# Kernel optimization log

Measured on AMD Instinct MI355X. Metric: run time of the kernel, lower is better.

Reference implementation:

```python
import jax, jax.numpy as jnp
import numpy as np

B, N, FEAT, HID = 1024, 128, 512, 256


def setup_inputs() -> dict:
    key = jax.random.key(0)
    k1, k2, k3, k4, k5, k6 = jax.random.split(key, 6)
    x = jax.random.normal(k1, (B, FEAT), dtype=jnp.float32)
    labels = jax.random.randint(k2, (B,), 0, N, dtype=jnp.int64)
    W_proj = jax.random.normal(k3, (FEAT, HID), dtype=jnp.float32) / np.sqrt(FEAT)
    b_proj = jax.random.normal(k4, (HID,), dtype=jnp.float32) * 0.01
    means = jax.random.normal(k5, (N, HID), dtype=jnp.float32)
    # inverse covariances must be SPD so sqrt(dist_sq) is real
    A = jax.random.normal(k6, (N, HID, HID), dtype=jnp.float32)
    inv_covs = jnp.einsum('nij,nkj->nik', A, A) / HID + 0.1 * jnp.eye(HID, dtype=jnp.float32)
    return {"x": x, "labels": labels, "W_proj": W_proj, "b_proj": b_proj,
            "means": means, "inv_covs": inv_covs}


def reference(x, labels, W_proj, b_proj, means, inv_covs):
    b = x.shape[0]
    n = means.shape[0]
    x_proj = x @ W_proj + b_proj                       # (b, hid)
    delta = x_proj[:, None, :] - means[None, :, :]     # (b, n, hid)
    # batched Mahalanobis quadratic form
    dist_sq = jnp.einsum('bni,nij,bnj->bn', delta, inv_covs, delta)
    distmat = jnp.sqrt(dist_sq + 1e-12)                # (b, n)
    center_mask = (labels[:, None] == jnp.arange(n)[None, :]).astype(distmat.dtype)
    loss = jnp.clip(distmat * center_mask, 1e-12, 1e12).sum() / b
    return loss, distmat
```

## Files before the change

kernel.cpp:

```cpp
#include <hip/hip_runtime.h>
#include <hip/hip_bf16.h>

#define B_    1024
#define N_    128
#define FEAT_ 512
#define HID_  256

typedef __bf16 bf16x8 __attribute__((ext_vector_type(8)));
typedef float  f32x4  __attribute__((ext_vector_type(4)));

__device__ __forceinline__ unsigned int f2bf(float f) {
    unsigned int u = __float_as_uint(f);
    u += 0x7fffu + ((u >> 16) & 1u);
    return u >> 16;
}
__device__ __forceinline__ unsigned int pack2(float a, float b) {
    return f2bf(a) | (f2bf(b) << 16);
}

__global__ __launch_bounds__(256) void prep_kernel(
    const float* __restrict__ x, const float* __restrict__ W,
    const float* __restrict__ bias, const float* __restrict__ means,
    const float* __restrict__ invcov,
    float* __restrict__ xp, unsigned short* __restrict__ xbf,
    unsigned short* __restrict__ Mbf, float* __restrict__ v2,
    float* __restrict__ cpart)
{
    const int t = threadIdx.x;
    if (blockIdx.x < 256) {
        __shared__ float xs[4][FEAT_];
        const int b0 = blockIdx.x * 4;
        {
            const float4* xsrc = (const float4*)(x + (size_t)b0 * FEAT_);
            const float4 v0 = xsrc[t];
            const float4 v1 = xsrc[t + 256];
            ((float4*)&xs[0][0])[t]       = v0;
            ((float4*)&xs[0][0])[t + 256] = v1;
        }
        __syncthreads();
        const int h = t;
        const float bb = bias[h];
        float a0 = bb, a1 = bb, a2 = bb, a3 = bb;
        #pragma unroll 8
        for (int f = 0; f < FEAT_; ++f) {
            const float w = W[(size_t)f * HID_ + h];
            a0 += xs[0][f] * w;
            a1 += xs[1][f] * w;
            a2 += xs[2][f] * w;
            a3 += xs[3][f] * w;
        }
        xp [(size_t)(b0 + 0) * HID_ + h] = a0;
        xp [(size_t)(b0 + 1) * HID_ + h] = a1;
        xp [(size_t)(b0 + 2) * HID_ + h] = a2;
        xp [(size_t)(b0 + 3) * HID_ + h] = a3;
        xbf[(size_t)(b0 + 0) * HID_ + h] = (unsigned short)f2bf(a0);
        xbf[(size_t)(b0 + 1) * HID_ + h] = (unsigned short)f2bf(a1);
        xbf[(size_t)(b0 + 2) * HID_ + h] = (unsigned short)f2bf(a2);
        xbf[(size_t)(b0 + 3) * HID_ + h] = (unsigned short)f2bf(a3);
    } else {
        __shared__ float sv[16][33];
        __shared__ float sw[2];
        const int cb = blockIdx.x - 256;
        const int n  = cb >> 4;
        const int jg = cb & 15;
        const float* Mn = invcov + (size_t)n * (HID_ * HID_) + (size_t)jg * 16 * HID_;
        const float* mu = means + (size_t)n * HID_;
        unsigned short* Mb = Mbf + (size_t)n * (HID_ * HID_) + (size_t)jg * 16 * HID_;
        const int gc = t & 31;
        const int r0 = t >> 5;
        const float4 mk0 = *(const float4*)(mu + gc * 8);
        const float4 mk1 = *(const float4*)(mu + gc * 8 + 4);
        #pragma unroll
        for (int i = 0; i < 2; ++i) {
            const int row = r0 + i * 8;
            const float* src = Mn + (size_t)row * HID_ + gc * 8;
            const float4 a = *(const float4*)src;
            const float4 b = *(const float4*)(src + 4);
            const int g2 = gc ^ ((row & 7) << 2);
            *(uint4*)(Mb + (size_t)row * HID_ + g2 * 8) =
                make_uint4(pack2(a.x, a.y), pack2(a.z, a.w), pack2(b.x, b.y), pack2(b.z, b.w));
            sv[row][gc] = a.x * mk0.x + a.y * mk0.y + a.z * mk0.z + a.w * mk0.w
                        + b.x * mk1.x + b.y * mk1.y + b.z * mk1.z + b.w * mk1.w;
        }
        __syncthreads();
        if (t < 128) {
            const int row = t >> 3;
            const int i0  = (t & 7) * 4;
            float v = sv[row][i0] + sv[row][i0 + 1] + sv[row][i0 + 2] + sv[row][i0 + 3];
            v += __shfl_xor(v, 1);
            v += __shfl_xor(v, 2);
            v += __shfl_xor(v, 4);
            const int j = jg * 16 + row;
            if ((t & 7) == 0) v2[(size_t)n * HID_ + j] = 2.f * v;
            float cc = ((t & 7) == 0) ? v * mu[j] : 0.f;
            cc += __shfl_xor(cc, 8);
            cc += __shfl_xor(cc, 16);
            cc += __shfl_xor(cc, 32);
            if ((t & 63) == 0) sw[t >> 6] = cc;
        }
        __syncthreads();
        if (t == 0) cpart[cb] = sw[0] + sw[1];
    }
}

__global__ __launch_bounds__(512, 4) void dist_kernel(
    const float* __restrict__ xp, const unsigned short* __restrict__ xbf,
    const unsigned short* __restrict__ Mbf, const float* __restrict__ v2,
    float* __restrict__ p)
{
    extern __shared__ unsigned short Ms[];

    const int tid  = threadIdx.x;
    const int bh   = blockIdx.x;
    const int jh   = blockIdx.y;
    const int n    = blockIdx.z;
    const int wave = tid >> 6;
    const int lane = tid & 63;
    const int q    = lane >> 4;
    const int l    = lane & 15;

    const unsigned short* src = Mbf + (size_t)n * (HID_ * HID_) + (size_t)jh * 32768;
    #pragma unroll
    for (int i = 0; i < 8; ++i) {
        const int c = i * 8 + wave;
        __builtin_amdgcn_global_load_lds(
            (const __attribute__((address_space(1))) unsigned int*)(src + (size_t)c * 512 + lane * 8),
            (__attribute__((address_space(3))) unsigned int*)&Ms[c * 512],
            16, 0, 0);
    }

    bf16x8 afrag[2][8];
    #pragma unroll
    for (int rb = 0; rb < 2; ++rb) {
        const unsigned short* xr = xbf + (size_t)(bh * 256 + wave * 32 + rb * 16 + l) * HID_;
        #pragma unroll
        for (int kk = 0; kk < 8; ++kk)
            afrag[rb][kk] = *(const bf16x8*)(xr + kk * 32 + q * 8);
    }
    float v2l[8];
    #pragma unroll
    for (int ct = 0; ct < 8; ++ct)
        v2l[ct] = v2[(size_t)n * HID_ + jh * 128 + ct * 16 + l];

    __syncthreads();

    float part[8];
    #pragma unroll
    for (int i = 0; i < 8; ++i) part[i] = 0.f;

    const size_t xbase = (size_t)(bh * 256 + wave * 32 + q * 4) * HID_ + jh * 128 + l;

    #pragma unroll
    for (int ct = 0; ct < 8; ++ct) {
        float xl[8];
        #pragma unroll
        for (int rb = 0; rb < 2; ++rb)
            #pragma unroll
            for (int r = 0; r < 4; ++r)
                xl[rb * 4 + r] = xp[xbase + (size_t)(rb * 16 + r) * HID_ + ct * 16];

        f32x4 acc0 = {0.f,0.f,0.f,0.f}, acc1 = {0.f,0.f,0.f,0.f};
        #pragma unroll
        for (int kk = 0; kk < 8; ++kk) {
            const bf16x8 bfrag = *(const bf16x8*)&Ms[(ct * 16 + l) * HID_ +
                                                     (((kk * 4 + q) ^ ((l & 7) << 2)) << 3)];
            acc0 = __builtin_amdgcn_mfma_f32_16x16x32_bf16(afrag[0][kk], bfrag, acc0, 0, 0, 0);
            acc1 = __builtin_amdgcn_mfma_f32_16x16x32_bf16(afrag[1][kk], bfrag, acc1, 0, 0, 0);
        }
        const float vv = v2l[ct];
        #pragma unroll
        for (int r = 0; r < 4; ++r) {
            part[r]     += (acc0[r] - vv) * xl[r];
            part[4 + r] += (acc1[r] - vv) * xl[4 + r];
        }
    }

    #pragma unroll
    for (int i = 0; i < 8; ++i) {
        float v = part[i];
        v += __shfl_xor(v, 1);
        v += __shfl_xor(v, 2);
        v += __shfl_xor(v, 4);
        v += __shfl_xor(v, 8);
        part[i] = v;
    }
    if (l == 0) {
        float* pb = p + (size_t)jh * (B_ * N_);
        #pragma unroll
        for (int i = 0; i < 8; ++i) {
            const int row = bh * 256 + wave * 32 + (i >> 2) * 16 + q * 4 + (i & 3);
            pb[(size_t)row * N_ + n] = part[i];
        }
    }
}

__global__ __launch_bounds__(256) void finalize_kernel(
    const float* __restrict__ p, const float* __restrict__ cpart,
    float* __restrict__ out)
{
    __shared__ float sc[128];
    const int t = threadIdx.x;
    if (t < 128) {
        float s = 0.f;
        #pragma unroll
        for (int g = 0; g < 16; ++g) s += cpart[t * 16 + g];
        sc[t] = s;
    }
    __syncthreads();
    const int i = blockIdx.x * 256 + t;
    const int n = i & (N_ - 1);
    out[1 + i] = sqrtf(p[i] + p[B_ * N_ + i] + sc[n] + 1e-12f);
}

__global__ __launch_bounds__(1024) void loss_kernel(
    const float* __restrict__ distmat, const int* __restrict__ labels,
    float* __restrict__ out)
{
    __shared__ float red[16];
    const int b = threadIdx.x;
    float s = distmat[(size_t)b * N_ + labels[b]];
    #pragma unroll
    for (int m = 1; m <= 32; m <<= 1) s += __shfl_xor(s, m);
    if ((b & 63) == 0) red[b >> 6] = s;
    __syncthreads();
    if (b == 0) {
        float t = 0.f;
        #pragma unroll
        for (int i = 0; i < 16; ++i) t += red[i];
        out[0] = t / (float)B_ + (float)(N_ - 1) * 1e-12f;
    }
}

extern "C" void kernel_launch(void* const* d_in, const int* in_sizes, int n_in,
                              void* d_out, int out_size, void* d_ws, size_t ws_size,
                              hipStream_t stream) {
    const float* x      = (const float*)d_in[0];
    const int*   labels = (const int*)d_in[1];
    const float* W      = (const float*)d_in[2];
    const float* bias   = (const float*)d_in[3];
    const float* means  = (const float*)d_in[4];
    const float* invcov = (const float*)d_in[5];
    float* out = (float*)d_out;

    char* ws = (char*)d_ws;
    unsigned short* Mbf   = (unsigned short*)(ws);
    float*          xp    = (float*)         (ws + 16777216);
    unsigned short* xbf   = (unsigned short*)(ws + 17825792);
    float*          v2    = (float*)         (ws + 18350080);
    float*          cpart = (float*)         (ws + 18481152);
    float*          p     = (float*)         (ws + 18489344);

    constexpr int DIST_LDS = 128 * HID_ * 2;
    (void)hipFuncSetAttribute((const void*)dist_kernel,
                              hipFuncAttributeMaxDynamicSharedMemorySize, DIST_LDS);

    prep_kernel<<<dim3(2304), 256, 0, stream>>>(x, W, bias, means, invcov,
                                                xp, xbf, Mbf, v2, cpart);
    dist_kernel<<<dim3(4, 2, N_), 512, DIST_LDS, stream>>>(xp, xbf, Mbf, v2, p);
    finalize_kernel<<<dim3((B_ * N_) / 256), 256, 0, stream>>>(p, cpart, out);
    loss_kernel<<<1, 1024, 0, stream>>>(out + 1, labels, out);
}
```

Measured before the change: 157.9 us.

## Fuse loss reduction into finalize, widen prep blocks and double-buffer projection loads

Removes the separate loss kernel: finalize now does the masked label sum per block and accumulates it into out[0] with atomicAdd, and prep seeds out[0] with the clip constant. The prep kernel moves to 512-thread blocks. The projection part handles 8 rows per block with float4 W loads double-buffered in registers, and the inv-cov conversion part processes 32 rows per block. This cuts one launch and should improve load efficiency in the projection, but float atomics make the loss summation order nondeterministic.

```diff
diff --git a/kernel.cpp b/kernel.cpp
--- a/kernel.cpp
+++ b/kernel.cpp
@@ -18,61 +18,77 @@
     return f2bf(a) | (f2bf(b) << 16);
 }
 
-__global__ __launch_bounds__(256) void prep_kernel(
+__global__ __launch_bounds__(512) void prep_kernel(
     const float* __restrict__ x, const float* __restrict__ W,
     const float* __restrict__ bias, const float* __restrict__ means,
     const float* __restrict__ invcov,
     float* __restrict__ xp, unsigned short* __restrict__ xbf,
     unsigned short* __restrict__ Mbf, float* __restrict__ v2,
-    float* __restrict__ cpart)
+    float* __restrict__ cpart, float* __restrict__ out)
 {
     const int t = threadIdx.x;
-    if (blockIdx.x < 256) {
-        __shared__ float xs[4][FEAT_];
-        const int b0 = blockIdx.x * 4;
+    if (blockIdx.x < 128) {
+        __shared__ float xs[8][FEAT_];
+        const int b0 = blockIdx.x * 8;
         {
             const float4* xsrc = (const float4*)(x + (size_t)b0 * FEAT_);
-            const float4 v0 = xsrc[t];
-            const float4 v1 = xsrc[t + 256];
-            ((float4*)&xs[0][0])[t]       = v0;
-            ((float4*)&xs[0][0])[t + 256] = v1;
-        }
+            ((float4*)&xs[0][0])[t]       = xsrc[t];
+            ((float4*)&xs[0][0])[t + 512] = xsrc[t + 512];
+        }
+        if (blockIdx.x == 0 && t == 0) out[0] = (float)(N_ - 1) * 1e-12f;
         __syncthreads();
-        const int h = t;
-        const float bb = bias[h];
-        float a0 = bb, a1 = bb, a2 = bb, a3 = bb;
-        #pragma unroll 8
-        for (int f = 0; f < FEAT_; ++f) {
-            const float w = W[(size_t)f * HID_ + h];
-            a0 += xs[0][f] * w;
-            a1 += xs[1][f] * w;
-            a2 += xs[2][f] * w;
-            a3 += xs[3][f] * w;
-        }
-        xp [(size_t)(b0 + 0) * HID_ + h] = a0;
-        xp [(size_t)(b0 + 1) * HID_ + h] = a1;
-        xp [(size_t)(b0 + 2) * HID_ + h] = a2;
-        xp [(size_t)(b0 + 3) * HID_ + h] = a3;
-        xbf[(size_t)(b0 + 0) * HID_ + h] = (unsigned short)f2bf(a0);
-        xbf[(size_t)(b0 + 1) * HID_ + h] = (unsigned short)f2bf(a1);
-        xbf[(size_t)(b0 + 2) * HID_ + h] = (unsigned short)f2bf(a2);
-        xbf[(size_t)(b0 + 3) * HID_ + h] = (unsigned short)f2bf(a3);
+        const int row = t >> 6;
+        const int h4  = t & 63;
+        const float* __restrict__ xr = &xs[row][0];
+        const float4* Wv = (const float4*)W;
+        float4 acc = ((const float4*)bias)[h4];
+        float4 Abuf[8], Bbuf[8];
+        auto LD = [&](float4 (&buf)[8], int g) {
+            #pragma unroll
+            for (int u = 0; u < 8; ++u) buf[u] = Wv[(size_t)(g * 8 + u) * 64 + h4];
+        };
+        auto FMA8 = [&](const float4 (&buf)[8], int g) {
+            const float4 xa = *(const float4*)(xr + g * 8);
+            const float4 xb = *(const float4*)(xr + g * 8 + 4);
+            const float xv[8] = {xa.x, xa.y, xa.z, xa.w, xb.x, xb.y, xb.z, xb.w};
+            #pragma unroll
+            for (int u = 0; u < 8; ++u) {
+                acc.x += xv[u] * buf[u].x;
+                acc.y += xv[u] * buf[u].y;
+                acc.z += xv[u] * buf[u].z;
+                acc.w += xv[u] * buf[u].w;
+            }
+        };
+        LD(Abuf, 0);
+        for (int g = 0; g < 62; g += 2) {
+            LD(Bbuf, g + 1);
+            FMA8(Abuf, g);
+            LD(Abuf, g + 2);
+            FMA8(Bbuf, g + 1);
+        }
+        LD(Bbuf, 63);
+        FMA8(Abuf, 62);
+        FMA8(Bbuf, 63);
+        const int gr = b0 + row;
+        ((float4*)(xp + (size_t)gr * HID_))[h4] = acc;
+        *(uint2*)(xbf + (size_t)gr * HID_ + h4 * 4) =
+            make_uint2(pack2(acc.x, acc.y), pack2(acc.z, acc.w));
     } else {
-        __shared__ float sv[16][33];
-        __shared__ float sw[2];
-        const int cb = blockIdx.x - 256;
-        const int n  = cb >> 4;
-        const int jg = cb & 15;
-        const float* Mn = invcov + (size_t)n * (HID_ * HID_) + (size_t)jg * 16 * HID_;
+        __shared__ float sv[32][33];
+        __shared__ float sw[4];
+        const int cb  = blockIdx.x - 128;
+        const int n   = cb >> 3;
+        const int jg2 = cb & 7;
+        const float* Mn = invcov + (size_t)n * (HID_ * HID_) + (size_t)jg2 * 32 * HID_;
         const float* mu = means + (size_t)n * HID_;
-        unsigned short* Mb = Mbf + (size_t)n * (HID_ * HID_) + (size_t)jg * 16 * HID_;
+        unsigned short* Mb = Mbf + (size_t)n * (HID_ * HID_) + (size_t)jg2 * 32 * HID_;
         const int gc = t & 31;
         const int r0 = t >> 5;
         const float4 mk0 = *(const float4*)(mu + gc * 8);
         const float4 mk1 = *(const float4*)(mu + gc * 8 + 4);
         #pragma unroll
         for (int i = 0; i < 2; ++i) {
-            const int row = r0 + i * 8;
+            const int row = r0 + i * 16;
             const float* src = Mn + (size_t)row * HID_ + gc * 8;
             const float4 a = *(const float4*)src;
             const float4 b = *(const float4*)(src + 4);
@@ -83,14 +99,14 @@
                         + b.x * mk1.x + b.y * mk1.y + b.z * mk1.z + b.w * mk1.w;
         }
         __syncthreads();
-        if (t < 128) {
+        if (t < 256) {
             const int row = t >> 3;
             const int i0  = (t & 7) * 4;
             float v = sv[row][i0] + sv[row][i0 + 1] + sv[row][i0 + 2] + sv[row][i0 + 3];
             v += __shfl_xor(v, 1);
             v += __shfl_xor(v, 2);
             v += __shfl_xor(v, 4);
-            const int j = jg * 16 + row;
+            const int j = jg2 * 32 + row;
             if ((t & 7) == 0) v2[(size_t)n * HID_ + j] = 2.f * v;
             float cc = ((t & 7) == 0) ? v * mu[j] : 0.f;
             cc += __shfl_xor(cc, 8);
@@ -99,7 +115,7 @@
             if ((t & 63) == 0) sw[t >> 6] = cc;
         }
         __syncthreads();
-        if (t == 0) cpart[cb] = sw[0] + sw[1];
+        if (t == 0) cpart[cb] = sw[0] + sw[1] + sw[2] + sw[3];
     }
 }
 
@@ -196,39 +212,29 @@
 
 __global__ __launch_bounds__(256) void finalize_kernel(
     const float* __restrict__ p, const float* __restrict__ cpart,
-    float* __restrict__ out)
+    const int* __restrict__ labels, float* __restrict__ out)
 {
     __shared__ float sc[128];
+    __shared__ float ls[4];
     const int t = threadIdx.x;
     if (t < 128) {
         float s = 0.f;
         #pragma unroll
-        for (int g = 0; g < 16; ++g) s += cpart[t * 16 + g];
+        for (int g = 0; g < 8; ++g) s += cpart[t * 8 + g];
         sc[t] = s;
     }
     __syncthreads();
     const int i = blockIdx.x * 256 + t;
     const int n = i & (N_ - 1);
-    out[1 + i] = sqrtf(p[i] + p[B_ * N_ + i] + sc[n] + 1e-12f);
-}
-
-__global__ __launch_bounds__(1024) void loss_kernel(
-    const float* __restrict__ distmat, const int* __restrict__ labels,
-    float* __restrict__ out)
-{
-    __shared__ float red[16];
-    const int b = threadIdx.x;
-    float s = distmat[(size_t)b * N_ + labels[b]];
-    #pragma unroll
-    for (int m = 1; m <= 32; m <<= 1) s += __shfl_xor(s, m);
-    if ((b & 63) == 0) red[b >> 6] = s;
+    const int b = i >> 7;
+    const float d = sqrtf(p[i] + p[B_ * N_ + i] + sc[n] + 1e-12f);
+    out[1 + i] = d;
+    float sel = (labels[b] == n) ? d : 0.f;
+    #pragma unroll
+    for (int m = 1; m <= 32; m <<= 1) sel += __shfl_xor(sel, m);
+    if ((t & 63) == 0) ls[t >> 6] = sel;
     __syncthreads();
-    if (b == 0) {
-        float t = 0.f;
-        #pragma unroll
-        for (int i = 0; i < 16; ++i) t += red[i];
-        out[0] = t / (float)B_ + (float)(N_ - 1) * 1e-12f;
-    }
+    if (t == 0) atomicAdd(out, (ls[0] + ls[1] + ls[2] + ls[3]) * (1.f / (float)B_));
 }
 
 extern "C" void kernel_launch(void* const* d_in, const int* in_sizes, int n_in,
@@ -254,9 +260,8 @@
     (void)hipFuncSetAttribute((const void*)dist_kernel,
                               hipFuncAttributeMaxDynamicSharedMemorySize, DIST_LDS);
 
-    prep_kernel<<<dim3(2304), 256, 0, stream>>>(x, W, bias, means, invcov,
-                                                xp, xbf, Mbf, v2, cpart);
+    prep_kernel<<<dim3(1152), 512, 0, stream>>>(x, W, bias, means, invcov,
+                                                xp, xbf, Mbf, v2, cpart, out);
     dist_kernel<<<dim3(4, 2, N_), 512, DIST_LDS, stream>>>(xp, xbf, Mbf, v2, p);
-    finalize_kernel<<<dim3((B_ * N_) / 256), 256, 0, stream>>>(p, cpart, out);
-    loss_kernel<<<1, 1024, 0, stream>>>(out + 1, labels, out);
-}
+    finalize_kernel<<<dim3((B_ * N_) / 256), 256, 0, stream>>>(p, cpart, labels, out);
+}
```

After: 200.8 us. 27.2% more time.
